# Optimization experiments

Hardware: AMD Instinct MI355X
Metric: run time of the kernel (lower is better)

## Reference

```python
import jax, jax.numpy as jnp
import numpy as np

B, N = 32, 512
N_DIM, N_P, N_K = 128, 3, 2
F0_DIM = N_DIM * N_P            # 384
CAT_DIM = N_DIM * (N_K + 1) * N_P  # 1152


def setup_inputs() -> dict:
    key = jax.random.key(0)
    ks = jax.random.split(key, 12)
    s = 0.05
    return {
        "loc": jax.random.uniform(ks[0], (B, N, 2), dtype=jnp.float32),
        "deadline": jax.random.uniform(ks[1], (B, N), dtype=jnp.float32),
        "workload": jax.random.uniform(ks[2], (B, N), dtype=jnp.float32),
        "depot": jax.random.uniform(ks[3], (B, 1, 2), dtype=jnp.float32),
        "W_init": jax.random.normal(ks[4], (3, F0_DIM), dtype=jnp.float32) * s,
        "b_init": jnp.zeros((F0_DIM,), jnp.float32),
        "W_dep": jax.random.normal(ks[5], (2, N_DIM), dtype=jnp.float32) * s,
        "b_dep": jnp.zeros((N_DIM,), jnp.float32),
        "W_g1": jax.random.normal(ks[6], (CAT_DIM, N_DIM), dtype=jnp.float32) * s,
        "b_g1": jnp.zeros((N_DIM,), jnp.float32),
        "W_g2": jax.random.normal(ks[7], (CAT_DIM, N_DIM), dtype=jnp.float32) * s,
        "b_g2": jnp.zeros((N_DIM,), jnp.float32),
        "W_g3": jax.random.normal(ks[8], (CAT_DIM, N_DIM), dtype=jnp.float32) * s,
        "b_g3": jnp.zeros((N_DIM,), jnp.float32),
        "gamma": jnp.ones((F0_DIM,), jnp.float32),
        "beta": jnp.zeros((F0_DIM,), jnp.float32),
        "W_F": jax.random.normal(ks[9], (F0_DIM, N_DIM), dtype=jnp.float32) * s,
        "b_F": jnp.zeros((N_DIM,), jnp.float32),
    }


def _forward(loc, deadline, workload, depot, W_init, b_init, W_dep, b_dep,
             W_g1, b_g1, W_g2, b_g2, W_g3, b_g3, gamma, beta, W_F, b_F):
    # X = [loc, deadline/deadline.max()] -> [B,N,3] (workload is concatenated then dropped in original)
    X = jnp.concatenate([loc, (deadline / deadline.max())[..., None]], axis=-1)
    n = X.shape[1]
    # pairwise squared distances [B,N,N]
    d2 = ((X[:, :, None, :] - X[:, None, :, :]) ** 2).sum(-1)
    off = ~jnp.eye(n, dtype=bool)                      # off-diagonal mask
    d2_safe = jnp.where(off, d2, 1.0)
    A = jnp.where(off, 1.0 / jnp.sqrt(d2_safe), 0.0)   # A = 1/dist off-diag, 0 on diag
    A = jnp.where(jnp.isnan(A), 0.0, A)                # A[A!=A]=0
    A = A / A.max()                                    # global max-normalize
    deg = A.sum(-1) - 1.0                              # (A.sum(-1) - 1)
    L = jnp.eye(n, dtype=A.dtype) * deg[:, None, :] - A  # D - A (diag = deg)
    L2 = L @ L

    F0 = X @ W_init + b_init                           # [B,N,384]
    F0_sq = F0 * F0
    F0_cu = F0 * F0_sq

    def prop(F):
        return jnp.concatenate([F, L @ F, L2 @ F], axis=-1)  # [B,N,1152]

    g1 = prop(F0) @ W_g1 + b_g1
    g2 = prop(F0_sq) @ W_g2 + b_g2
    g3 = prop(F0_cu) @ W_g3 + b_g3
    F1 = jnp.concatenate([g1, g2, g3], axis=-1)        # [B,N,384]
    F1 = jax.nn.leaky_relu(F1) + F0

    # BatchNorm1d (training mode): stats over flattened (B*N) samples, biased var
    flat = F1.reshape(-1, F1.shape[-1])
    mu = flat.mean(0)
    var = ((flat - mu) ** 2).mean(0)
    F1 = (F1 - mu) / jnp.sqrt(var + 1e-5) * gamma + beta

    F_final = jax.nn.leaky_relu(F1 @ W_F + b_F)        # [B,N,128]
    dep = depot @ W_dep + b_dep                        # [B,1,128]
    h = jnp.concatenate([dep, F_final], axis=1)        # [B,N+1,128]
    return h, h.mean(axis=1)


def reference(loc, deadline, workload, depot, W_init, b_init, W_dep, b_dep,
              W_g1, b_g1, W_g2, b_g2, W_g3, b_g3, gamma, beta, W_F, b_F):
    return _forward(loc, deadline, workload, depot, W_init, b_init, W_dep, b_dep,
                    W_g1, b_g1, W_g2, b_g2, W_g3, b_g3, gamma, beta, W_F, b_F)
```

## Files before the change

### kernel.cpp

```cpp
#include <hip/hip_runtime.h>

#define LEAKY(x) ((x) > 0.0f ? (x) : 0.01f * (x))

typedef __attribute__((ext_vector_type(8))) short bf16x8;
typedef __attribute__((ext_vector_type(4))) float f32x4;
typedef __attribute__((ext_vector_type(8))) unsigned short u16x8;
typedef __attribute__((ext_vector_type(4))) unsigned short u16x4;

__device__ __forceinline__ unsigned short f2bf(float f) {
    unsigned int u = __float_as_uint(f);
    unsigned int r = (u + 0x7fffu + ((u >> 16) & 1u)) >> 16;
    return (unsigned short)r;
}
__device__ __forceinline__ float bf2f(unsigned short u) {
    return __uint_as_float(((unsigned int)u) << 16);
}

#define GLD16(gp, lp) __builtin_amdgcn_global_load_lds( \
    (__attribute__((address_space(1))) void*)(gp), \
    (__attribute__((address_space(3))) void*)(lp), 16, 0, 0)


__global__ void k_dmax(const float* __restrict__ deadline, float* __restrict__ dmax) {
    int t = threadIdx.x;
    float m = deadline[blockIdx.x * 256 + t];
    for (int off = 32; off > 0; off >>= 1) m = fmaxf(m, __shfl_down(m, off));
    __shared__ float s[4];
    if ((t & 63) == 0) s[t >> 6] = m;
    __syncthreads();
    if (t == 0) atomicMax((unsigned int*)dmax,
                          __float_as_uint(fmaxf(fmaxf(s[0], s[1]), fmaxf(s[2], s[3]))));
}

__global__ __launch_bounds__(256) void k_rowstats(const float* __restrict__ loc,
                                                  const float* __restrict__ deadline,
                                                  const float* __restrict__ dmaxv,
                                                  float* __restrict__ rowsum, float* __restrict__ pmax64) {
    int blk = blockIdx.x;
    int wave = threadIdx.x >> 6, lane = threadIdx.x & 63;
    int bi = blk * 4 + wave;
    int b = bi >> 9, i = bi & 511;
    float invd = 1.0f / (*dmaxv);
    const float* lb = loc + b * 1024;
    const float* db = deadline + b * 512;
    float xi = lb[i * 2], yi = lb[i * 2 + 1], zi = db[i] * invd;
    float lsum = 0.f, lmax = 0.f;
    for (int j = lane; j < 512; j += 64) {
        float d0 = xi - lb[j * 2], d1 = yi - lb[j * 2 + 1], d2 = zi - db[j] * invd;
        float dd = d0 * d0 + d1 * d1 + d2 * d2;
        float r = (j == i) ? 0.f : rsqrtf(dd);
        lsum += r; lmax = fmaxf(lmax, r);
    }
    for (int off = 32; off > 0; off >>= 1) {
        lsum += __shfl_down(lsum, off);
        lmax = fmaxf(lmax, __shfl_down(lmax, off));
    }
    __shared__ float smax[4];
    if (lane == 0) { rowsum[bi] = lsum; smax[wave] = lmax; }
    __syncthreads();
    if (threadIdx.x == 0) {
        float m = fmaxf(fmaxf(smax[0], smax[1]), fmaxf(smax[2], smax[3]));
        atomicMax((unsigned int*)(pmax64 + (blk & 63)), __float_as_uint(m));
    }
}

__global__ __launch_bounds__(256) void k_build(
    const float* __restrict__ loc, const float* __restrict__ deadline,
    const float* __restrict__ dmaxv, const float* __restrict__ rowsum,
    const float* __restrict__ pmax64,
    const float* __restrict__ Wi, const float* __restrict__ bi_,
    const float* __restrict__ Wg1, const float* __restrict__ Wg2, const float* __restrict__ Wg3,
    unsigned short* __restrict__ Lb,
    unsigned short* __restrict__ P1, unsigned short* __restrict__ P2, unsigned short* __restrict__ P3,
    unsigned short* __restrict__ WgT)
{
    __shared__ float amaxS;
    int blk = blockIdx.x;
    int t = threadIdx.x;
    if (blk < 8192) {
        if (t < 64) {
            float m = pmax64[t];
            for (int off = 32; off > 0; off >>= 1) m = fmaxf(m, __shfl_down(m, off));
            if (t == 0) amaxS = m;
        }
        __syncthreads();
        float inv = 1.0f / amaxS;
        float invd = 1.0f / (*dmaxv);
        int id = blk * 256 + t;
        size_t e = (size_t)id * 4;
        size_t bi = e >> 9;
        int b = (int)(bi >> 9);
        int i = (int)(bi & 511);
        int j0 = (int)(e & 511);
        const float* lb = loc + b * 1024;
        const float* db = deadline + b * 512;
        float xi = lb[i * 2], yi = lb[i * 2 + 1], zi = db[i] * invd;
        float4 l01 = *(const float4*)(lb + j0 * 2);
        float4 l23 = *(const float4*)(lb + j0 * 2 + 4);
        float4 dj = *(const float4*)(db + j0);
        float diag = rowsum[bi] * inv - 1.0f;
        float jx[4] = {l01.x, l01.z, l23.x, l23.z};
        float jy[4] = {l01.y, l01.w, l23.y, l23.w};
        float jz[4] = {dj.x * invd, dj.y * invd, dj.z * invd, dj.w * invd};
        u16x4 o;
#pragma unroll
        for (int j = 0; j < 4; j++) {
            float d0 = xi - jx[j], d1 = yi - jy[j], d2 = zi - jz[j];
            float dd = d0 * d0 + d1 * d1 + d2 * d2;
            float v = (i == j0 + j) ? diag : -rsqrtf(dd) * inv;
            o[j] = f2bf(v);
        }
        *(u16x4*)(Lb + e) = o;
    } else if (blk < 14336) {
        int id = (blk - 8192) * 256 + t;
        int row = id / 96, c4 = (id % 96) * 4;
        float x0 = loc[row * 2], x1 = loc[row * 2 + 1], x2 = deadline[row] / (*dmaxv);
        float4 w0 = *(const float4*)(Wi + c4);
        float4 w1 = *(const float4*)(Wi + 384 + c4);
        float4 w2 = *(const float4*)(Wi + 768 + c4);
        float4 bb = *(const float4*)(bi_ + c4);
        float f[4] = {x0 * w0.x + x1 * w1.x + x2 * w2.x + bb.x,
                      x0 * w0.y + x1 * w1.y + x2 * w2.y + bb.y,
                      x0 * w0.z + x1 * w1.z + x2 * w2.z + bb.z,
                      x0 * w0.w + x1 * w1.w + x2 * w2.w + bb.w};
        u16x4 o1, o2, o3;
#pragma unroll
        for (int j = 0; j < 4; j++) {
            o1[j] = f2bf(f[j]); o2[j] = f2bf(f[j] * f[j]); o3[j] = f2bf(f[j] * f[j] * f[j]);
        }
        size_t e = (size_t)row * 384 + c4;
        *(u16x4*)(P1 + e) = o1; *(u16x4*)(P2 + e) = o2; *(u16x4*)(P3 + e) = o3;
    } else {
        int id = (blk - 14336) * 256 + t;
        int part = id / 147456, rem = id % 147456;
        int g = rem / 384, k = rem % 384;
        int kp = g >> 7, n = g & 127;
        const float* W = (kp == 0) ? Wg1 : (kp == 1 ? Wg2 : Wg3);
        WgT[id] = f2bf(W[(part * 384 + k) * 128 + n]);
    }
}


__device__ __forceinline__ void pipe128x128(
    const unsigned short* __restrict__ A0, int As0, const unsigned short* __restrict__ B0, int Bs0, int it0,
    const unsigned short* __restrict__ A1, int As1, const unsigned short* __restrict__ B1, int Bs1, int it1,
    unsigned short* AsL, unsigned short* BsL,
    f32x4 (&acc)[4][4], int t)
{
    const int lane = t & 63, wave = t >> 6;
    const int wm = wave >> 1, wn = wave & 1;
    const int quad = lane >> 4, l16 = lane & 15;
    const int lrow = lane >> 3;
    const int lsw  = ((lane & 7) ^ lrow) * 8;
    const int total = it0 + it1;

    auto stage = [&](int buf, const unsigned short* A, int As,
                     const unsigned short* B, int Bs, int k0) {
#pragma unroll
        for (int j = 0; j < 4; j++) {
            int r0 = wave * 32 + j * 8;
            GLD16(A + (size_t)(r0 + lrow) * As + k0 + lsw, AsL + buf * 8192 + r0 * 64);
            GLD16(B + (size_t)(r0 + lrow) * Bs + k0 + lsw, BsL + buf * 8192 + r0 * 64);
        }
    };

    stage(0, A0, As0, B0, Bs0, 0);
    int buf = 0;
    for (int s = 0; s < total; s++) {
        __syncthreads();
        if (s + 1 < total) {
            int s2 = s + 1;
            int sg = (s2 >= it0);
            int k0 = (sg ? (s2 - it0) : s2) * 64;
            stage(buf ^ 1, sg ? A1 : A0, sg ? As1 : As0,
                            sg ? B1 : B0, sg ? Bs1 : Bs0, k0);
        }
#pragma unroll
        for (int h = 0; h < 2; h++) {
            bf16x8 af[4], bfr[4];
            int phys = ((h * 4 + quad) ^ (l16 & 7)) * 8;
#pragma unroll
            for (int i = 0; i < 4; i++)
                af[i] = *(const bf16x8*)(AsL + buf * 8192 + (wm * 64 + i * 16 + l16) * 64 + phys);
#pragma unroll
            for (int n = 0; n < 4; n++)
                bfr[n] = *(const bf16x8*)(BsL + buf * 8192 + (wn * 64 + n * 16 + l16) * 64 + phys);
#pragma unroll
            for (int i = 0; i < 4; i++)
#pragma unroll
                for (int n = 0; n < 4; n++)
                    acc[i][n] = __builtin_amdgcn_mfma_f32_16x16x32_bf16(af[i], bfr[n], acc[i][n], 0, 0, 0);
        }
        buf ^= 1;
    }
}

__device__ __forceinline__ void pipe64x64(
    const unsigned short* __restrict__ A0, int As0, const unsigned short* __restrict__ B0, int Bs0, int it0,
    unsigned short* AsL, unsigned short* BsL,
    f32x4 (&acc)[2][2], int t)
{
    const int lane = t & 63, wave = t >> 6;
    const int wm = wave >> 1, wn = wave & 1;
    const int quad = lane >> 4, l16 = lane & 15;
    const int lrow = lane >> 3;
    const int lsw  = ((lane & 7) ^ lrow) * 8;

    auto stage = [&](int buf, int k0) {
#pragma unroll
        for (int j = 0; j < 2; j++) {
            int r0 = wave * 16 + j * 8;
            GLD16(A0 + (size_t)(r0 + lrow) * As0 + k0 + lsw, AsL + buf * 4096 + r0 * 64);
            GLD16(B0 + (size_t)(r0 + lrow) * Bs0 + k0 + lsw, BsL + buf * 4096 + r0 * 64);
        }
    };

    stage(0, 0);
    int buf = 0;
    for (int s = 0; s < it0; s++) {
        __syncthreads();
        if (s + 1 < it0) stage(buf ^ 1, (s + 1) * 64);
#pragma unroll
        for (int h = 0; h < 2; h++) {
            bf16x8 af[2], bfr[2];
            int phys = ((h * 4 + quad) ^ (l16 & 7)) * 8;
#pragma unroll
            for (int i = 0; i < 2; i++)
                af[i] = *(const bf16x8*)(AsL + buf * 4096 + (wm * 32 + i * 16 + l16) * 64 + phys);
#pragma unroll
            for (int n = 0; n < 2; n++)
                bfr[n] = *(const bf16x8*)(BsL + buf * 4096 + (wn * 32 + n * 16 + l16) * 64 + phys);
#pragma unroll
            for (int i = 0; i < 2; i++)
#pragma unroll
                for (int n = 0; n < 2; n++)
                    acc[i][n] = __builtin_amdgcn_mfma_f32_16x16x32_bf16(af[i], bfr[n], acc[i][n], 0, 0, 0);
        }
        buf ^= 1;
    }
}

__global__ __launch_bounds__(256) void k_ygemmT(
    const unsigned short* __restrict__ WgT,
    const unsigned short* __restrict__ P1, const unsigned short* __restrict__ P2,
    const unsigned short* __restrict__ P3, unsigned short* __restrict__ Y2T)
{
    __shared__ unsigned short AsL[16384], BsL[16384];
    const int t = threadIdx.x;
    const int id = blockIdx.x;
    const int b = id & 31, tt = id >> 5;
    const int kp = tt >> 2, nb = tt & 3;
    const unsigned short* P = (kp == 0) ? P1 : (kp == 1 ? P2 : P3);
    f32x4 acc[4][4];
#pragma unroll
    for (int i = 0; i < 4; i++)
#pragma unroll
        for (int n = 0; n < 4; n++) acc[i][n] = (f32x4){0.f, 0.f, 0.f, 0.f};
    pipe128x128(WgT + ((size_t)2 * 384 + kp * 128) * 384, 384,
                P + ((size_t)b * 512 + nb * 128) * 384, 384, 6,
                nullptr, 0, nullptr, 0, 0, AsL, BsL, acc, t);

    const int wave = t >> 6, lane = t & 63;
    const int wm = wave >> 1, wn = wave & 1;
    const int quad = lane >> 4, l16 = lane & 15;
#pragma unroll
    for (int i = 0; i < 4; i++)
#pragma unroll
        for (int n = 0; n < 4; n++) {
            int g = kp * 128 + wm * 64 + i * 16 + quad * 4;
            int node = nb * 128 + wn * 64 + n * 16 + l16;
#pragma unroll
            for (int r = 0; r < 4; r++)
                Y2T[((size_t)b * 384 + g + r) * 512 + node] = f2bf(acc[i][n][r]);
        }
}

__global__ __launch_bounds__(256) void k_lg1T(
    const unsigned short* __restrict__ Lb, const unsigned short* __restrict__ Y2T,
    const unsigned short* __restrict__ WgT,
    const unsigned short* __restrict__ P1, const unsigned short* __restrict__ P2,
    const unsigned short* __restrict__ P3, unsigned short* __restrict__ ZT)
{
    __shared__ unsigned short AsL[16384], BsL[16384];
    const int t = threadIdx.x;
    const int id = blockIdx.x;
    const int b = id & 31, tt = id >> 5;
    const int kp = tt >> 2, nb = tt & 3;
    const unsigned short* P = (kp == 0) ? P1 : (kp == 1 ? P2 : P3);
    f32x4 acc[4][4];
#pragma unroll
    for (int i = 0; i < 4; i++)
#pragma unroll
        for (int n = 0; n < 4; n++) acc[i][n] = (f32x4){0.f, 0.f, 0.f, 0.f};
    pipe128x128(Y2T + (size_t)b * 196608 + (size_t)kp * 128 * 512, 512,
                Lb + (size_t)b * 262144 + (size_t)nb * 128 * 512, 512, 8,
                WgT + ((size_t)1 * 384 + kp * 128) * 384, 384,
                P + ((size_t)b * 512 + nb * 128) * 384, 384, 6, AsL, BsL, acc, t);

    const int wave = t >> 6, lane = t & 63;
    const int wm = wave >> 1, wn = wave & 1;
    const int quad = lane >> 4, l16 = lane & 15;
#pragma unroll
    for (int i = 0; i < 4; i++)
#pragma unroll
        for (int n = 0; n < 4; n++) {
            int g = kp * 128 + wm * 64 + i * 16 + quad * 4;
            int node = nb * 128 + wn * 64 + n * 16 + l16;
#pragma unroll
            for (int r = 0; r < 4; r++)
                ZT[((size_t)b * 384 + g + r) * 512 + node] = f2bf(acc[i][n][r]);
        }
}

__global__ __launch_bounds__(256) void k_lg2(
    const unsigned short* __restrict__ Lb, const unsigned short* __restrict__ ZT,
    const unsigned short* __restrict__ WgT,
    const unsigned short* __restrict__ P1, const unsigned short* __restrict__ P2,
    const unsigned short* __restrict__ P3,
    const float* __restrict__ bg1, const float* __restrict__ bg2, const float* __restrict__ bg3,
    unsigned short* __restrict__ F1b, float* __restrict__ bn1, float* __restrict__ bn2)
{
    __shared__ unsigned short AsL[16384], BsL[16384];
    __shared__ float bnS[128], bnQ[128];
    const int t = threadIdx.x;
    const int id = blockIdx.x;
    const int b = id & 31, tt = id >> 5;
    const int mb = tt & 3, gt = tt >> 2;
    if (t < 128) { bnS[t] = 0.f; bnQ[t] = 0.f; }
    const unsigned short* P = (gt == 0) ? P1 : (gt == 1 ? P2 : P3);
    f32x4 acc[4][4];
#pragma unroll
    for (int i = 0; i < 4; i++)
#pragma unroll
        for (int n = 0; n < 4; n++) acc[i][n] = (f32x4){0.f, 0.f, 0.f, 0.f};
    pipe128x128(Lb + (size_t)b * 262144 + (size_t)mb * 128 * 512, 512,
                ZT + (size_t)b * 196608 + (size_t)gt * 128 * 512, 512, 8,
                P + ((size_t)b * 512 + mb * 128) * 384, 384,
                WgT + (size_t)(gt * 128) * 384, 384, 6,
                AsL, BsL, acc, t);

    const int wave = t >> 6, lane = t & 63;
    const int wm = wave >> 1, wn = wave & 1;
    const int quad = lane >> 4, l16 = lane & 15;
    const float* bg = (gt == 0) ? bg1 : (gt == 1 ? bg2 : bg3);
    float ls1[4], ls2[4];
#pragma unroll
    for (int n = 0; n < 4; n++) { ls1[n] = 0.f; ls2[n] = 0.f; }
#pragma unroll
    for (int i = 0; i < 4; i++) {
        int rowl = mb * 128 + wm * 64 + i * 16 + quad * 4;
        size_t rowg = (size_t)b * 512 + rowl;
#pragma unroll
        for (int n = 0; n < 4; n++) {
            int nloc = wn * 64 + n * 16 + l16;
            int g = gt * 128 + nloc;
            float bias = bg[nloc];
#pragma unroll
            for (int r = 0; r < 4; r++) {
                size_t idx = (rowg + r) * 384 + g;
                float c = acc[i][n][r] + bias;
                float v = LEAKY(c) + bf2f(P1[idx]);
                F1b[idx] = f2bf(v);
                ls1[n] += v; ls2[n] += v * v;
            }
        }
    }
#pragma unroll
    for (int n = 0; n < 4; n++) {
        int nloc = wn * 64 + n * 16 + l16;
        atomicAdd(&bnS[nloc], ls1[n]);
        atomicAdd(&bnQ[nloc], ls2[n]);
    }
    __syncthreads();
    if (t < 128) {
        atomicAdd(&bn1[gt * 128 + t], bnS[t]);
        atomicAdd(&bn2[gt * 128 + t], bnQ[t]);
    }
}

__global__ __launch_bounds__(256) void k_bnfold(
    const float* __restrict__ bn1, const float* __restrict__ bn2,
    const float* __restrict__ gamma, const float* __restrict__ beta,
    const float* __restrict__ WF, const float* __restrict__ bF,
    unsigned short* __restrict__ WFsT, float* __restrict__ beffv)
{
    int blk = blockIdx.x;
    if (blk < 192) {
        int id = blk * 256 + threadIdx.x;
        int n = id / 384, k = id % 384;
        float mu = bn1[k] * (1.f / 16384.f);
        float var = bn2[k] * (1.f / 16384.f) - mu * mu;
        float sc = gamma[k] / sqrtf(var + 1e-5f);
        WFsT[id] = f2bf(WF[k * 128 + n] * sc);
    } else {
        __shared__ float ttL[384];
        int c = threadIdx.x;
        for (int k = c; k < 384; k += 256) {
            float mu = bn1[k] * (1.f / 16384.f);
            float var = bn2[k] * (1.f / 16384.f) - mu * mu;
            float sc = gamma[k] / sqrtf(var + 1e-5f);
            ttL[k] = beta[k] - mu * sc;
        }
        __syncthreads();
        if (c < 128) {
            float a = bF[c];
            for (int k = 0; k < 384; k++) a += ttL[k] * WF[k * 128 + c];
            beffv[c] = a;
        }
    }
}

__global__ __launch_bounds__(256) void k_fgemm(
    const unsigned short* __restrict__ F1b, const unsigned short* __restrict__ WFsT,
    const float* __restrict__ beffv, float* __restrict__ out, float* __restrict__ msum)
{
    __shared__ unsigned short AsL[8192], BsL[8192];
    __shared__ float msS[64];
    const int t = threadIdx.x;
    const int id = blockIdx.x;
    const int b = id & 31, tt = id >> 5;
    const int seg = tt >> 1, nt = tt & 1;
    if (t < 64) msS[t] = 0.f;
    f32x4 acc[2][2];
#pragma unroll
    for (int i = 0; i < 2; i++)
#pragma unroll
        for (int n = 0; n < 2; n++) acc[i][n] = (f32x4){0.f, 0.f, 0.f, 0.f};
    pipe64x64(F1b + ((size_t)b * 512 + seg * 64) * 384, 384,
              WFsT + (size_t)nt * 64 * 384, 384, 6, AsL, BsL, acc, t);

    const int wave = t >> 6, lane = t & 63;
    const int wm = wave >> 1, wn = wave & 1;
    const int quad = lane >> 4, l16 = lane & 15;
    float ls[2];
#pragma unroll
    for (int n = 0; n < 2; n++) ls[n] = 0.f;
#pragma unroll
    for (int i = 0; i < 2; i++) {
        int nd = seg * 64 + wm * 32 + i * 16 + quad * 4;
#pragma unroll
        for (int n = 0; n < 2; n++) {
            int col = nt * 64 + wn * 32 + n * 16 + l16;
            float bb = beffv[col];
#pragma unroll
            for (int r = 0; r < 4; r++) {
                float x = acc[i][n][r] + bb;
                float v = LEAKY(x);
                out[(size_t)b * 65664 + (size_t)(nd + r + 1) * 128 + col] = v;
                ls[n] += v;
            }
        }
    }
#pragma unroll
    for (int n = 0; n < 2; n++) atomicAdd(&msS[wn * 32 + n * 16 + l16], ls[n]);
    __syncthreads();
    if (t < 64) atomicAdd(&msum[b * 128 + nt * 64 + t], msS[t]);
}

__global__ void k_meandep(const float* __restrict__ depot, const float* __restrict__ Wd,
                          const float* __restrict__ bd, const float* __restrict__ msum,
                          float* __restrict__ out) {
    int id = blockIdx.x * 256 + threadIdx.x;
    int b = id >> 7, o = id & 127;
    float dep = depot[b * 2] * Wd[o] + depot[b * 2 + 1] * Wd[128 + o] + bd[o];
    out[(size_t)b * 65664 + o] = dep;
    out[2101248 + id] = (msum[id] + dep) * (1.0f / 513.0f);
}


extern "C" void kernel_launch(void* const* d_in, const int* in_sizes, int n_in,
                              void* d_out, int out_size, void* d_ws, size_t ws_size,
                              hipStream_t stream) {
    const float* loc      = (const float*)d_in[0];
    const float* deadline = (const float*)d_in[1];
    const float* depot    = (const float*)d_in[3];
    const float* W_init   = (const float*)d_in[4];
    const float* b_init   = (const float*)d_in[5];
    const float* W_dep    = (const float*)d_in[6];
    const float* b_dep    = (const float*)d_in[7];
    const float* W_g1     = (const float*)d_in[8];
    const float* b_g1     = (const float*)d_in[9];
    const float* W_g2     = (const float*)d_in[10];
    const float* b_g2     = (const float*)d_in[11];
    const float* W_g3     = (const float*)d_in[12];
    const float* b_g3     = (const float*)d_in[13];
    const float* gamma    = (const float*)d_in[14];
    const float* beta     = (const float*)d_in[15];
    const float* W_F      = (const float*)d_in[16];
    const float* b_F      = (const float*)d_in[17];
    float* out = (float*)d_out;
    float* ws  = (float*)d_ws;

    float* dmaxv  = ws + 0;
    float* pmax64 = ws + 4;
    float* bn1    = ws + 68;
    float* bn2    = ws + 452;
    float* msum   = ws + 836;
    float* rowsum = ws + 4932;
    float* beffv  = ws + 21316;
    unsigned short* Lb   = (unsigned short*)(ws + 21448);
    unsigned short* P1   = (unsigned short*)(ws + 4215752);
    unsigned short* P2   = (unsigned short*)(ws + 7361480);
    unsigned short* P3   = (unsigned short*)(ws + 10507208);
    unsigned short* WgT  = (unsigned short*)(ws + 13652936);
    unsigned short* WFsT = (unsigned short*)(ws + 13874120);
    unsigned short* Y2T  = (unsigned short*)(ws + 13898696);
    unsigned short* ZT   = (unsigned short*)(ws + 17044424);
    unsigned short* F1b  = (unsigned short*)(ws + 20190152);

    hipMemsetAsync(ws, 0, 4932 * sizeof(float), stream);

    k_dmax<<<64, 256, 0, stream>>>(deadline, dmaxv);
    k_rowstats<<<4096, 256, 0, stream>>>(loc, deadline, dmaxv, rowsum, pmax64);
    k_build<<<16064, 256, 0, stream>>>(loc, deadline, dmaxv, rowsum, pmax64,
                                       W_init, b_init, W_g1, W_g2, W_g3,
                                       Lb, P1, P2, P3, WgT);

    k_ygemmT<<<384, 256, 0, stream>>>(WgT, P1, P2, P3, Y2T);
    k_lg1T<<<384, 256, 0, stream>>>(Lb, Y2T, WgT, P1, P2, P3, ZT);
    k_lg2<<<384, 256, 0, stream>>>(Lb, ZT, WgT, P1, P2, P3,
                                   b_g1, b_g2, b_g3, F1b, bn1, bn2);

    k_bnfold<<<193, 256, 0, stream>>>(bn1, bn2, gamma, beta, W_F, b_F, WFsT, beffv);
    k_fgemm<<<512, 256, 0, stream>>>(F1b, WFsT, beffv, out, msum);
    k_meandep<<<16, 256, 0, stream>>>(depot, W_dep, b_dep, msum, out);
}
```

Baseline: 241.4 us.

## Prefetch two stages ahead with explicit vmcnt waits in GEMM pipelines

Both GEMM main loops now issue global-to-LDS loads two k-steps ahead instead of one. Each step waits only on the older stage with an explicit s_waitcnt vmcnt, reads the whole tile from LDS into registers, and then hits a second barrier. After that barrier it refills the just-freed buffer while the MFMAs run from registers. The aim is to hide global load latency behind compute, at the cost of an extra barrier per iteration and more live registers for the fragments.

```diff
diff --git a/kernel.cpp b/kernel.cpp
--- a/kernel.cpp
+++ b/kernel.cpp
@@ -154,8 +154,12 @@
     const int lsw  = ((lane & 7) ^ lrow) * 8;
     const int total = it0 + it1;
 
-    auto stage = [&](int buf, const unsigned short* A, int As,
-                     const unsigned short* B, int Bs, int k0) {
+    auto stage = [&](int buf, int s) {
+        int sg = (s >= it0);
+        const unsigned short* A = sg ? A1 : A0;
+        const unsigned short* B = sg ? B1 : B0;
+        int As = sg ? As1 : As0, Bs = sg ? Bs1 : Bs0;
+        int k0 = (sg ? (s - it0) : s) * 64;
 #pragma unroll
         for (int j = 0; j < 4; j++) {
             int r0 = wave * 32 + j * 8;
@@ -164,34 +168,37 @@
         }
     };
 
-    stage(0, A0, As0, B0, Bs0, 0);
-    int buf = 0;
+    stage(0, 0);
+    if (total > 1) stage(1, 1);
     for (int s = 0; s < total; s++) {
-        __syncthreads();
-        if (s + 1 < total) {
-            int s2 = s + 1;
-            int sg = (s2 >= it0);
-            int k0 = (sg ? (s2 - it0) : s2) * 64;
-            stage(buf ^ 1, sg ? A1 : A0, sg ? As1 : As0,
-                            sg ? B1 : B0, sg ? Bs1 : Bs0, k0);
-        }
+        const int buf = s & 1;
+        if (s + 1 < total) asm volatile("s_waitcnt vmcnt(8)" ::: "memory");
+        else               asm volatile("s_waitcnt vmcnt(0)" ::: "memory");
+        __builtin_amdgcn_s_barrier();
+        __builtin_amdgcn_sched_barrier(0);
+        bf16x8 af[2][4], bfr[2][4];
 #pragma unroll
         for (int h = 0; h < 2; h++) {
-            bf16x8 af[4], bfr[4];
             int phys = ((h * 4 + quad) ^ (l16 & 7)) * 8;
 #pragma unroll
             for (int i = 0; i < 4; i++)
-                af[i] = *(const bf16x8*)(AsL + buf * 8192 + (wm * 64 + i * 16 + l16) * 64 + phys);
+                af[h][i] = *(const bf16x8*)(AsL + buf * 8192 + (wm * 64 + i * 16 + l16) * 64 + phys);
 #pragma unroll
             for (int n = 0; n < 4; n++)
-                bfr[n] = *(const bf16x8*)(BsL + buf * 8192 + (wn * 64 + n * 16 + l16) * 64 + phys);
+                bfr[h][n] = *(const bf16x8*)(BsL + buf * 8192 + (wn * 64 + n * 16 + l16) * 64 + phys);
+        }
+        asm volatile("s_waitcnt lgkmcnt(0)" ::: "memory");
+        __builtin_amdgcn_sched_barrier(0);
+        __builtin_amdgcn_s_barrier();
+        __builtin_amdgcn_sched_barrier(0);
+        if (s + 2 < total) stage(buf, s + 2);
+#pragma unroll
+        for (int h = 0; h < 2; h++)
 #pragma unroll
             for (int i = 0; i < 4; i++)
 #pragma unroll
                 for (int n = 0; n < 4; n++)
-                    acc[i][n] = __builtin_amdgcn_mfma_f32_16x16x32_bf16(af[i], bfr[n], acc[i][n], 0, 0, 0);
-        }
-        buf ^= 1;
+                    acc[i][n] = __builtin_amdgcn_mfma_f32_16x16x32_bf16(af[h][i], bfr[h][n], acc[i][n], 0, 0, 0);
     }
 }
 
@@ -206,7 +213,8 @@
     const int lrow = lane >> 3;
     const int lsw  = ((lane & 7) ^ lrow) * 8;
 
-    auto stage = [&](int buf, int k0) {
+    auto stage = [&](int buf, int s) {
+        int k0 = s * 64;
 #pragma unroll
         for (int j = 0; j < 2; j++) {
             int r0 = wave * 16 + j * 8;
@@ -216,27 +224,36 @@
     };
 
     stage(0, 0);
-    int buf = 0;
+    if (it0 > 1) stage(1, 1);
     for (int s = 0; s < it0; s++) {
-        __syncthreads();
-        if (s + 1 < it0) stage(buf ^ 1, (s + 1) * 64);
+        const int buf = s & 1;
+        if (s + 1 < it0) asm volatile("s_waitcnt vmcnt(4)" ::: "memory");
+        else             asm volatile("s_waitcnt vmcnt(0)" ::: "memory");
+        __builtin_amdgcn_s_barrier();
+        __builtin_amdgcn_sched_barrier(0);
+        bf16x8 af[2][2], bfr[2][2];
 #pragma unroll
         for (int h = 0; h < 2; h++) {
-            bf16x8 af[2], bfr[2];
             int phys = ((h * 4 + quad) ^ (l16 & 7)) * 8;
 #pragma unroll
             for (int i = 0; i < 2; i++)
-                af[i] = *(const bf16x8*)(AsL + buf * 4096 + (wm * 32 + i * 16 + l16) * 64 + phys);
+                af[h][i] = *(const bf16x8*)(AsL + buf * 4096 + (wm * 32 + i * 16 + l16) * 64 + phys);
 #pragma unroll
             for (int n = 0; n < 2; n++)
-                bfr[n] = *(const bf16x8*)(BsL + buf * 4096 + (wn * 32 + n * 16 + l16) * 64 + phys);
+                bfr[h][n] = *(const bf16x8*)(BsL + buf * 4096 + (wn * 32 + n * 16 + l16) * 64 + phys);
+        }
+        asm volatile("s_waitcnt lgkmcnt(0)" ::: "memory");
+        __builtin_amdgcn_sched_barrier(0);
+        __builtin_amdgcn_s_barrier();
+        __builtin_amdgcn_sched_barrier(0);
+        if (s + 2 < it0) stage(buf, s + 2);
+#pragma unroll
+        for (int h = 0; h < 2; h++)
 #pragma unroll
             for (int i = 0; i < 2; i++)
 #pragma unroll
                 for (int n = 0; n < 2; n++)
-                    acc[i][n] = __builtin_amdgcn_mfma_f32_16x16x32_bf16(af[i], bfr[n], acc[i][n], 0, 0, 0);
-        }
-        buf ^= 1;
+                    acc[i][n] = __builtin_amdgcn_mfma_f32_16x16x32_bf16(af[h][i], bfr[h][n], acc[i][n], 0, 0, 0);
     }
 }
 
```

Result: faster. 222.6 us (median of 2 runs) (-7.8%).
